# Kernel optimization log

Measured on AMD Instinct MI355X. Metric: run time of the kernel, lower is better.

Reference implementation:

```python
import jax, jax.numpy as jnp
import numpy as np

# physical constants / config (from __init__ defaults + chosen kwargs)
WFA_C = 4.6686e-13   # e/(4*pi*m_e*c) in 1/(G*Angstrom)
LAMBDA0 = 6301.5     # Angstrom
G_FACTOR = 1.5
WFA_WEIGHT = 0.5
STOKES_V = 3
BLOS_THRESH = 100.0
BASE_THRESH = 0.0004
TAU_IDX = np.array([0, 1, 2])
N_LOGTAU, N_MAGS = 21, 4
NWL = 112
START, END = 0, NWL - 1  # wavelength_range=None -> [0, len-1) slice
EPS = 1e-10


def _np_gradient(x):
    """np.gradient along last axis: central diffs interior, one-sided edges."""
    left = x[..., 1:2] - x[..., 0:1]
    mid = (x[..., 2:] - x[..., :-2]) * 0.5
    right = x[..., -1:] - x[..., -2:-1]
    return jnp.concatenate([left, mid, right], axis=-1)


def setup_inputs() -> dict:
    key = jax.random.key(0)
    kS, kP, kT = jax.random.split(key, 3)
    B = 65536
    input_stokes = jax.random.normal(kS, (B, 4, NWL), dtype=jnp.float32) * 0.01
    predicted_atm = jax.random.normal(kP, (B, N_LOGTAU * N_MAGS), dtype=jnp.float32)
    # target close to prediction so base MAE < base_loss_threshold -> WFA branch active
    target_atm = predicted_atm + 1e-4 * jax.random.normal(kT, (B, N_LOGTAU * N_MAGS), dtype=jnp.float32)
    wavelengths = jnp.linspace(6300.5, 6303.0, NWL).astype(jnp.float32)
    return {"input_stokes": input_stokes, "predicted_atm": predicted_atm,
            "target_atm": target_atm, "wavelengths": wavelengths}


def reference(input_stokes, predicted_atm, target_atm, wavelengths):
    # base MAE loss
    base_loss = jnp.mean(jnp.abs(predicted_atm - target_atm))

    # --- WFA B_LOS estimate, vectorized over batch ---
    wl = wavelengths[START:END]                      # [L]
    I = input_stokes[:, 0, START:END]                # [B, L]
    V = input_stokes[:, STOKES_V, START:END]         # [B, L]
    dI = _np_gradient(I) / _np_gradient(wl)[None, :]  # dI/dlambda, [B, L]

    # least squares V ~ p0*dI + p1; 2-column pinv == closed-form normal equations
    n = jnp.float32(dI.shape[-1])
    sd = jnp.sum(dI, axis=-1)
    sv = jnp.sum(V, axis=-1)
    sdd = jnp.sum(dI * dI, axis=-1)
    sdv = jnp.sum(dI * V, axis=-1)
    p0 = (n * sdv - sd * sv) / (n * sdd - sd * sd)   # slope, [B]
    wfa_blos = -p0 / (WFA_C * LAMBDA0 ** 2 * G_FACTOR)  # Gauss, [B]

    # predicted B_LOS: mean over tau_indices of last magnetic parameter
    atm = predicted_atm.reshape(-1, N_LOGTAU, N_MAGS)
    predicted_blos = atm[:, TAU_IDX, -1].mean(axis=1)  # [B]

    # thresholded masked log-abs MAE
    mask = jnp.abs(wfa_blos) < BLOS_THRESH
    diff = jnp.abs(jnp.log10(jnp.abs(predicted_blos) + EPS)
                   - jnp.log10(jnp.abs(wfa_blos) + EPS))
    cnt = jnp.sum(mask)
    wfa_loss_masked = jnp.sum(jnp.where(mask, diff, 0.0)) / jnp.maximum(cnt, 1).astype(diff.dtype)

    # early-return semantics: WFA only if base_loss < threshold AND any mask
    apply_wfa = (base_loss < BASE_THRESH) & (cnt > 0)
    wfa_loss = jnp.where(apply_wfa, wfa_loss_masked, jnp.float32(0.0))
    total_loss = jnp.where(apply_wfa,
                           (1.0 - WFA_WEIGHT) * base_loss + WFA_WEIGHT * wfa_loss_masked,
                           base_loss)
    return total_loss, base_loss, wfa_loss
```

## Files before the change

kernel.cpp:

```cpp
#include <hip/hip_runtime.h>
#include <math.h>

#define NWL   112
#define NCOLS 111
#define NATM  84
#define THREADS 256
#define WAVES_PER_BLOCK 4
#define MAIN_BLOCKS 2048

typedef float f4v __attribute__((ext_vector_type(4)));

template<int CTRL>
__device__ __forceinline__ float dpp_add(float v) {
    int x = __builtin_amdgcn_update_dpp(0, __float_as_int(v), CTRL, 0xF, 0xF, true);
    return v + __int_as_float(x);
}

__device__ __forceinline__ float half_reduce_sum(float v) {
    v = dpp_add<0xB1>(v);
    v = dpp_add<0x4E>(v);
    v = dpp_add<0x124>(v);
    v = dpp_add<0x128>(v);
    v = dpp_add<0x142>(v);
    return v;
}

__device__ __forceinline__ float wave_reduce_sum(float v) {
#pragma unroll
    for (int off = 32; off >= 1; off >>= 1)
        v += __shfl_xor(v, off, 64);
    return v;
}

__global__ __launch_bounds__(THREADS) void wfa_main(
    const float* __restrict__ stokes,
    const float* __restrict__ pred,
    const float* __restrict__ targ,
    const float* __restrict__ wl,
    float* __restrict__ ws,
    int nrows, int nblocks)
{
    __shared__ float s_idw[NWL];
    __shared__ float s_red[WAVES_PER_BLOCK][3];

    const int tid  = threadIdx.x;
    const int lane = tid & 63;
    const int wid  = tid >> 6;
    const int sub  = lane & 31;
    const int g    = lane & 32;

    if (tid < NWL) {
        const int j = tid;
        float d;
        if (j == 0)              d = wl[1] - wl[0];
        else if (j == NCOLS - 1) d = wl[NCOLS - 1] - wl[NCOLS - 2];
        else if (j < NCOLS - 1)  d = 0.5f * (wl[j + 1] - wl[j - 1]);
        else                     d = 1.0f;
        s_idw[j] = (j == NCOLS) ? 0.0f : 1.0f / d;
    }
    __syncthreads();

    float4 idw4 = make_float4(0.f, 0.f, 0.f, 0.f);
    if (sub < 28) idw4 = *(const float4*)&s_idw[4 * sub];

    const float WFA_DEN = (float)(4.6686e-13 * 6301.5 * 6301.5 * 1.5);

    const int h  = (blockIdx.x * WAVES_PER_BLOCK + wid) * 2 + (lane >> 5);
    const int nh = nblocks * WAVES_PER_BLOCK * 2;

    float base_acc = 0.f;
    float wfa_acc  = 0.f;
    float cnt_acc  = 0.f;

    for (int r = h; r < nrows; r += nh) {
        const float* rowbase = stokes + (size_t)r * (4 * NWL);

        float4 I4 = make_float4(0.f, 0.f, 0.f, 0.f);
        float4 V4 = make_float4(0.f, 0.f, 0.f, 0.f);
        if (sub < 28) {
            f4v iv = __builtin_nontemporal_load((const f4v*)rowbase + sub);
            f4v vv = __builtin_nontemporal_load((const f4v*)(rowbase + 3 * NWL) + sub);
            I4 = make_float4(iv.x, iv.y, iv.z, iv.w);
            V4 = make_float4(vv.x, vv.y, vv.z, vv.w);
        }

        float4 P4 = make_float4(0.f, 0.f, 0.f, 0.f);
        float bpart = 0.f;
        if (sub < 21) {
            f4v pv = __builtin_nontemporal_load((const f4v*)(pred + (size_t)r * NATM) + sub);
            f4v tv = __builtin_nontemporal_load((const f4v*)(targ + (size_t)r * NATM) + sub);
            P4 = make_float4(pv.x, pv.y, pv.z, pv.w);
            bpart = fabsf(pv.x - tv.x) + fabsf(pv.y - tv.y)
                  + fabsf(pv.z - tv.z) + fabsf(pv.w - tv.w);
        }
        base_acc += bpart;

        const int lm1 = lane - (sub ? 1 : 0);
        const float im1 = __shfl(I4.w, lm1, 64);
        const float ip4 = __shfl(I4.x, lane + 1, 64);
        const float a3  = __shfl(P4.w, g | 0, 64);
        const float a7  = __shfl(P4.w, g | 1, 64);
        const float a11 = __shfl(P4.w, g | 2, 64);

        const float n0 = (sub == 0)  ? (I4.y - I4.x) : 0.5f * (I4.y - im1);
        const float n1 = 0.5f * (I4.z - I4.x);
        const float n2 = (sub == 27) ? (I4.z - I4.y) : 0.5f * (I4.w - I4.y);
        const float n3 = 0.5f * (ip4 - I4.z);

        const float d0 = n0 * idw4.x;
        const float d1 = n1 * idw4.y;
        const float d2 = n2 * idw4.z;
        const float d3 = n3 * idw4.w;
        const float v3 = (sub == 27) ? 0.f : V4.w;

        float sd  = d0 + d1 + d2 + d3;
        float sdd = fmaf(d0, d0, fmaf(d1, d1, fmaf(d2, d2, d3 * d3)));
        float sdv = fmaf(d0, V4.x, fmaf(d1, V4.y, fmaf(d2, V4.z, d3 * v3)));
        float sv  = V4.x + V4.y + V4.z + v3;

        sd  = half_reduce_sum(sd);
        sdd = half_reduce_sum(sdd);
        sdv = half_reduce_sum(sdv);
        sv  = half_reduce_sum(sv);

        if (sub == 16) {
            const float n  = (float)NCOLS;
            const float p0 = (n * sdv - sd * sv) / (n * sdd - sd * sd);
            const float ab = fabsf(p0) / WFA_DEN;
            if (ab < 100.0f) {
                const float pb = (a3 + a7 + a11) / 3.0f;
                wfa_acc += fabsf(log10f(fabsf(pb) + 1e-10f) - log10f(ab + 1e-10f));
                cnt_acc += 1.0f;
            }
        }
    }

    base_acc = wave_reduce_sum(base_acc);
    wfa_acc  = wave_reduce_sum(wfa_acc);
    cnt_acc  = wave_reduce_sum(cnt_acc);
    if (lane == 0) {
        s_red[wid][0] = base_acc;
        s_red[wid][1] = wfa_acc;
        s_red[wid][2] = cnt_acc;
    }
    __syncthreads();
    if (tid == 0) {
        float b = 0.f, w = 0.f, c = 0.f;
#pragma unroll
        for (int k = 0; k < WAVES_PER_BLOCK; ++k) {
            b += s_red[k][0]; w += s_red[k][1]; c += s_red[k][2];
        }
        ws[blockIdx.x]               = b;
        ws[nblocks + blockIdx.x]     = w;
        ws[2 * nblocks + blockIdx.x] = c;
    }
}

__global__ __launch_bounds__(256) void wfa_final(
    const float* __restrict__ ws, float* __restrict__ out,
    int nblocks, int nrows)
{
    const int tid = threadIdx.x;
    float b = 0.f, w = 0.f, c = 0.f;
    for (int i = tid; i < nblocks; i += 256) {
        b += ws[i];
        w += ws[nblocks + i];
        c += ws[2 * nblocks + i];
    }
    b = wave_reduce_sum(b);
    w = wave_reduce_sum(w);
    c = wave_reduce_sum(c);

    __shared__ float sb[4], sw[4], sc[4];
    const int lane = tid & 63, wid = tid >> 6;
    if (lane == 0) { sb[wid] = b; sw[wid] = w; sc[wid] = c; }
    __syncthreads();
    if (tid == 0) {
        const float B_ = sb[0] + sb[1] + sb[2] + sb[3];
        const float W_ = sw[0] + sw[1] + sw[2] + sw[3];
        const float C_ = sc[0] + sc[1] + sc[2] + sc[3];
        const float base_loss = B_ / (float)((long long)nrows * NATM);
        const float wfa_ml    = W_ / fmaxf(C_, 1.0f);
        const bool  apply     = (base_loss < 0.0004f) && (C_ > 0.f);
        out[0] = apply ? (0.5f * base_loss + 0.5f * wfa_ml) : base_loss;
        out[1] = base_loss;
        out[2] = apply ? wfa_ml : 0.f;
    }
}

extern "C" void kernel_launch(void* const* d_in, const int* in_sizes, int n_in,
                              void* d_out, int out_size, void* d_ws, size_t ws_size,
                              hipStream_t stream)
{
    const float* stokes = (const float*)d_in[0];
    const float* pred   = (const float*)d_in[1];
    const float* targ   = (const float*)d_in[2];
    const float* wl     = (const float*)d_in[3];
    float* out = (float*)d_out;
    float* ws  = (float*)d_ws;

    const int nrows = in_sizes[1] / NATM;

    int nblocks = MAIN_BLOCKS;
    const size_t need = (size_t)nblocks * 3 * sizeof(float);
    if (ws_size < need) {
        nblocks = (int)(ws_size / (3 * sizeof(float)));
        if (nblocks < 1) nblocks = 1;
    }

    hipLaunchKernelGGL(wfa_main, dim3(nblocks), dim3(THREADS), 0, stream,
                       stokes, pred, targ, wl, ws, nrows, nblocks);
    hipLaunchKernelGGL(wfa_final, dim3(1), dim3(256), 0, stream,
                       ws, out, nblocks, nrows);
}
```

Measured before the change: 187.2 us.

## Process one row per half-wave with loads issued before shared setup

After: 188.1 us. About the same (+0.5%).

```diff
diff --git a/kernel.cpp b/kernel.cpp
--- a/kernel.cpp
+++ b/kernel.cpp
@@ -6,7 +6,7 @@
 #define NATM  84
 #define THREADS 256
 #define WAVES_PER_BLOCK 4
-#define MAIN_BLOCKS 2048
+#define ROWS_PER_BLOCK 8
 
 typedef float f4v __attribute__((ext_vector_type(4)));
 
@@ -49,6 +49,27 @@
     const int sub  = lane & 31;
     const int g    = lane & 32;
 
+    const int r = blockIdx.x * ROWS_PER_BLOCK + wid * 2 + (lane >> 5);
+    const bool live = (r < nrows);
+
+    float4 I4 = make_float4(0.f, 0.f, 0.f, 0.f);
+    float4 V4 = make_float4(0.f, 0.f, 0.f, 0.f);
+    float4 P4 = make_float4(0.f, 0.f, 0.f, 0.f);
+    float4 T4 = make_float4(0.f, 0.f, 0.f, 0.f);
+    if (live && sub < 28) {
+        const float* rowbase = stokes + (size_t)r * (4 * NWL);
+        f4v iv = __builtin_nontemporal_load((const f4v*)rowbase + sub);
+        f4v vv = __builtin_nontemporal_load((const f4v*)(rowbase + 3 * NWL) + sub);
+        I4 = make_float4(iv.x, iv.y, iv.z, iv.w);
+        V4 = make_float4(vv.x, vv.y, vv.z, vv.w);
+    }
+    if (live && sub < 21) {
+        f4v pv = __builtin_nontemporal_load((const f4v*)(pred + (size_t)r * NATM) + sub);
+        f4v tv = __builtin_nontemporal_load((const f4v*)(targ + (size_t)r * NATM) + sub);
+        P4 = make_float4(pv.x, pv.y, pv.z, pv.w);
+        T4 = make_float4(tv.x, tv.y, tv.z, tv.w);
+    }
+
     if (tid < NWL) {
         const int j = tid;
         float d;
@@ -65,73 +86,49 @@
 
     const float WFA_DEN = (float)(4.6686e-13 * 6301.5 * 6301.5 * 1.5);
 
-    const int h  = (blockIdx.x * WAVES_PER_BLOCK + wid) * 2 + (lane >> 5);
-    const int nh = nblocks * WAVES_PER_BLOCK * 2;
-
     float base_acc = 0.f;
     float wfa_acc  = 0.f;
     float cnt_acc  = 0.f;
 
-    for (int r = h; r < nrows; r += nh) {
-        const float* rowbase = stokes + (size_t)r * (4 * NWL);
-
-        float4 I4 = make_float4(0.f, 0.f, 0.f, 0.f);
-        float4 V4 = make_float4(0.f, 0.f, 0.f, 0.f);
-        if (sub < 28) {
-            f4v iv = __builtin_nontemporal_load((const f4v*)rowbase + sub);
-            f4v vv = __builtin_nontemporal_load((const f4v*)(rowbase + 3 * NWL) + sub);
-            I4 = make_float4(iv.x, iv.y, iv.z, iv.w);
-            V4 = make_float4(vv.x, vv.y, vv.z, vv.w);
-        }
-
-        float4 P4 = make_float4(0.f, 0.f, 0.f, 0.f);
-        float bpart = 0.f;
-        if (sub < 21) {
-            f4v pv = __builtin_nontemporal_load((const f4v*)(pred + (size_t)r * NATM) + sub);
-            f4v tv = __builtin_nontemporal_load((const f4v*)(targ + (size_t)r * NATM) + sub);
-            P4 = make_float4(pv.x, pv.y, pv.z, pv.w);
-            bpart = fabsf(pv.x - tv.x) + fabsf(pv.y - tv.y)
-                  + fabsf(pv.z - tv.z) + fabsf(pv.w - tv.w);
-        }
-        base_acc += bpart;
-
-        const int lm1 = lane - (sub ? 1 : 0);
-        const float im1 = __shfl(I4.w, lm1, 64);
-        const float ip4 = __shfl(I4.x, lane + 1, 64);
-        const float a3  = __shfl(P4.w, g | 0, 64);
-        const float a7  = __shfl(P4.w, g | 1, 64);
-        const float a11 = __shfl(P4.w, g | 2, 64);
-
-        const float n0 = (sub == 0)  ? (I4.y - I4.x) : 0.5f * (I4.y - im1);
-        const float n1 = 0.5f * (I4.z - I4.x);
-        const float n2 = (sub == 27) ? (I4.z - I4.y) : 0.5f * (I4.w - I4.y);
-        const float n3 = 0.5f * (ip4 - I4.z);
-
-        const float d0 = n0 * idw4.x;
-        const float d1 = n1 * idw4.y;
-        const float d2 = n2 * idw4.z;
-        const float d3 = n3 * idw4.w;
-        const float v3 = (sub == 27) ? 0.f : V4.w;
-
-        float sd  = d0 + d1 + d2 + d3;
-        float sdd = fmaf(d0, d0, fmaf(d1, d1, fmaf(d2, d2, d3 * d3)));
-        float sdv = fmaf(d0, V4.x, fmaf(d1, V4.y, fmaf(d2, V4.z, d3 * v3)));
-        float sv  = V4.x + V4.y + V4.z + v3;
-
-        sd  = half_reduce_sum(sd);
-        sdd = half_reduce_sum(sdd);
-        sdv = half_reduce_sum(sdv);
-        sv  = half_reduce_sum(sv);
-
-        if (sub == 16) {
-            const float n  = (float)NCOLS;
-            const float p0 = (n * sdv - sd * sv) / (n * sdd - sd * sd);
-            const float ab = fabsf(p0) / WFA_DEN;
-            if (ab < 100.0f) {
-                const float pb = (a3 + a7 + a11) / 3.0f;
-                wfa_acc += fabsf(log10f(fabsf(pb) + 1e-10f) - log10f(ab + 1e-10f));
-                cnt_acc += 1.0f;
-            }
+    base_acc = fabsf(P4.x - T4.x) + fabsf(P4.y - T4.y)
+             + fabsf(P4.z - T4.z) + fabsf(P4.w - T4.w);
+
+    const int lm1 = lane - (sub ? 1 : 0);
+    const float im1 = __shfl(I4.w, lm1, 64);
+    const float ip4 = __shfl(I4.x, lane + 1, 64);
+    const float a3  = __shfl(P4.w, g | 0, 64);
+    const float a7  = __shfl(P4.w, g | 1, 64);
+    const float a11 = __shfl(P4.w, g | 2, 64);
+
+    const float n0 = (sub == 0)  ? (I4.y - I4.x) : 0.5f * (I4.y - im1);
+    const float n1 = 0.5f * (I4.z - I4.x);
+    const float n2 = (sub == 27) ? (I4.z - I4.y) : 0.5f * (I4.w - I4.y);
+    const float n3 = 0.5f * (ip4 - I4.z);
+
+    const float d0 = n0 * idw4.x;
+    const float d1 = n1 * idw4.y;
+    const float d2 = n2 * idw4.z;
+    const float d3 = n3 * idw4.w;
+    const float v3 = (sub == 27) ? 0.f : V4.w;
+
+    float sd  = d0 + d1 + d2 + d3;
+    float sdd = fmaf(d0, d0, fmaf(d1, d1, fmaf(d2, d2, d3 * d3)));
+    float sdv = fmaf(d0, V4.x, fmaf(d1, V4.y, fmaf(d2, V4.z, d3 * v3)));
+    float sv  = V4.x + V4.y + V4.z + v3;
+
+    sd  = half_reduce_sum(sd);
+    sdd = half_reduce_sum(sdd);
+    sdv = half_reduce_sum(sdv);
+    sv  = half_reduce_sum(sv);
+
+    if (live && sub == 16) {
+        const float n  = (float)NCOLS;
+        const float p0 = (n * sdv - sd * sv) / (n * sdd - sd * sd);
+        const float ab = fabsf(p0) / WFA_DEN;
+        if (ab < 100.0f) {
+            const float pb = (a3 + a7 + a11) / 3.0f;
+            wfa_acc += fabsf(log10f(fabsf(pb) + 1e-10f) - log10f(ab + 1e-10f));
+            cnt_acc += 1.0f;
         }
     }
 
@@ -201,10 +198,10 @@
 
     const int nrows = in_sizes[1] / NATM;
 
-    int nblocks = MAIN_BLOCKS;
-    const size_t need = (size_t)nblocks * 3 * sizeof(float);
-    if (ws_size < need) {
-        nblocks = (int)(ws_size / (3 * sizeof(float)));
+    int nblocks = (nrows + ROWS_PER_BLOCK - 1) / ROWS_PER_BLOCK;
+    const size_t cap = ws_size / (3 * sizeof(float));
+    if ((size_t)nblocks > cap) {
+        nblocks = (int)cap;
         if (nblocks < 1) nblocks = 1;
     }
 
```
